# Kernel optimization log

Hardware: AMD Instinct MI355X
Metric: run time of the kernel (lower is better)

## Reference

```python
import jax, jax.numpy as jnp
import numpy as np

TEMPERATURE = 0.07
EPS = 1e-8  # torch CosineSimilarity eps


def setup_inputs() -> dict:
    key = jax.random.key(0)
    features = jax.random.normal(key, (16, 1024, 512), dtype=jnp.float32)
    return {"features": features}


def reference(features):
    """Vectorized equivalent of the original double Python loop.

    For each b and each t in [1, T-2]:
      anchor = f[b,t], positive = f[b,t+1]
      negatives = all frames j with j < t-1 or j >= t+2  (excludes t-1, t, t+1)
      loss_bt = -log( exp(cos(a,p)/T) / (exp(cos(a,p)/T) + sum_j exp(cos(a,n_j)/T)) )
    Returns mean over all (b, t) pairs (neg pool is non-empty for all t when T > 3).
    """
    B, T, D = features.shape
    norm = jnp.maximum(jnp.linalg.norm(features, axis=-1, keepdims=True), EPS)
    n = features / norm  # [B, T, D]
    # full pairwise cosine-sim logits, scaled by temperature
    sim = jnp.einsum('btd,bsd->bts', n, n) / TEMPERATURE  # [B, T, T]

    t_idx = jnp.arange(1, T - 1)            # anchors t = 1 .. T-2
    j_idx = jnp.arange(T)
    # negatives: j in [0, t-1) union [t+2, T)  -> excludes t-1, t, t+1
    neg_mask = (j_idx[None, :] < t_idx[:, None] - 1) | (j_idx[None, :] >= t_idx[:, None] + 2)  # [T-2, T]

    logits = sim[:, 1:T - 1, :]                                   # [B, T-2, T]
    pos = logits[:, jnp.arange(T - 2), jnp.arange(2, T)]          # sim[b, t, t+1] -> [B, T-2]
    neg_logits = jnp.where(neg_mask[None], logits, -jnp.inf)
    lse_neg = jax.nn.logsumexp(neg_logits, axis=-1)               # log sum_j exp(neg_sim)
    # -log(exp(pos)/(exp(pos)+negsum)) = logaddexp(pos, lse_neg) - pos
    loss_bt = jnp.logaddexp(pos, lse_neg) - pos                   # [B, T-2]
    return jnp.mean(loss_bt)
```

## Files before the change

kernel.cpp:

```cpp
#include <hip/hip_runtime.h>
#include <hip/hip_bf16.h>
#include <hip/hip_fp8.h>

#define B_ 16
#define T_ 1024
#define D_ 512
#define EPS_ 1e-8f
#define SCALE2 20.609929155566063f
#define LN2_ 0.6931471805599453f

#define BT 64
#define NB 16
#define NPAIR (NB * (NB + 1) / 2)
#define NKIT 4
#define SCL 0x7B7B7B7B

typedef __attribute__((ext_vector_type(4))) int   int4v;
typedef __attribute__((ext_vector_type(8))) int   int8v;
typedef __attribute__((ext_vector_type(4))) float floatx4;

typedef __attribute__((address_space(1))) const unsigned int g_u32;
typedef __attribute__((address_space(3))) unsigned int l_u32;

__device__ __forceinline__ void glds16(const void* g, void* l) {
    __builtin_amdgcn_global_load_lds((g_u32*)g, (l_u32*)l, 16, 0, 0);
}

__device__ __forceinline__ unsigned char f2e4m3(float x) {
    __hip_fp8_e4m3 q(x);
    return (unsigned char)q.__x;
}

__global__ __launch_bounds__(256) void norm_kernel(const float* __restrict__ f,
                                                   unsigned char* __restrict__ nrm,
                                                   float* __restrict__ rs_g,
                                                   float* __restrict__ rp_g,
                                                   float* __restrict__ out) {
    const int gi = blockIdx.x * 256 + threadIdx.x;
    if (gi < B_ * T_) { rs_g[gi] = 0.0f; rp_g[gi] = 0.0f; }
    if (gi == 0) out[0] = 0.0f;

    const int row  = blockIdx.x * 4 + (threadIdx.x >> 6);
    const int lane = threadIdx.x & 63;
    const size_t off = (size_t)row * D_ + lane * 8;
    const float4 v0 = *(const float4*)(f + off);
    const float4 v1 = *(const float4*)(f + off + 4);
    float ss = v0.x*v0.x + v0.y*v0.y + v0.z*v0.z + v0.w*v0.w
             + v1.x*v1.x + v1.y*v1.y + v1.z*v1.z + v1.w*v1.w;
    #pragma unroll
    for (int o = 32; o >= 1; o >>= 1) ss += __shfl_xor(ss, o, 64);
    const float sc = 16.0f / fmaxf(sqrtf(ss), EPS_);
    unsigned int w0 =  (unsigned int)f2e4m3(v0.x*sc)
                    | ((unsigned int)f2e4m3(v0.y*sc) << 8)
                    | ((unsigned int)f2e4m3(v0.z*sc) << 16)
                    | ((unsigned int)f2e4m3(v0.w*sc) << 24);
    unsigned int w1 =  (unsigned int)f2e4m3(v1.x*sc)
                    | ((unsigned int)f2e4m3(v1.y*sc) << 8)
                    | ((unsigned int)f2e4m3(v1.z*sc) << 16)
                    | ((unsigned int)f2e4m3(v1.w*sc) << 24);
    uint2 w; w.x = w0; w.y = w1;
    *(uint2*)(nrm + (size_t)row * D_ + lane * 8) = w;
}

__global__ __launch_bounds__(64) void loss_kernel(const unsigned char* __restrict__ nrm,
                                                  float* __restrict__ rs_g,
                                                  float* __restrict__ rp_g) {
    const int slot = blockIdx.x & 15;
    int u = blockIdx.x >> 4;
    const int b = ((slot & 7) << 1) | (slot >> 3);
    int bi = 0, rem = NB;
    while (u >= rem) { u -= rem; --rem; ++bi; }
    const int bj   = bi + u;
    const bool diag = (bi == bj);
    const bool near = (bj - bi) <= 1;

    const int t0 = bi * BT;
    const int j0 = bj * BT;
    const char* base = (const char*)(nrm + (size_t)b * T_ * D_);

    __shared__ __align__(16) char Ar[4][4096];
    __shared__ __align__(16) char Br[4][4096];

    const int l = threadIdx.x & 63;
    const int m = l & 15;

    const int r   = l >> 2;
    const int gsw = (l & 3) ^ ((r >> 1) & 3);
    const char* sA[4];
    const char* sB[4];
    #pragma unroll
    for (int i = 0; i < 4; ++i) {
        sA[i] = base + (size_t)(t0 + i * 16 + r) * 512 + gsw * 16;
        sB[i] = base + (size_t)(j0 + i * 16 + r) * 512 + gsw * 16;
    }

#define ISSUE(S) do {                                                  \
    _Pragma("unroll")                                                  \
    for (int i_ = 0; i_ < 4; ++i_)                                     \
        glds16(sA[i_] + (S) * 64, Ar[(S) & 3] + i_ * 1024);            \
    if (!diag) {                                                       \
        _Pragma("unroll")                                              \
        for (int i_ = 0; i_ < 4; ++i_)                                 \
            glds16(sB[i_] + (S) * 64, Br[(S) & 3] + i_ * 1024);        \
    }                                                                  \
} while (0)

    const int kqh  = l >> 5;
    const int ph0  = (2 * ((l >> 4) & 1)) ^ ((m >> 1) & 3);
    const int rd0  = m * 64 + ph0 * 16;
    const int rd1  = m * 64 + (ph0 ^ 1) * 16;

    floatx4 acc[4][4] = {};

    ISSUE(0); ISSUE(1);

    #pragma unroll
    for (int j = 0; j < NKIT; ++j) {
        __syncthreads();
        if (j < NKIT - 1) { ISSUE(2 * j + 2); ISSUE(2 * j + 3); }

        const char* As = Ar[(2 * j + kqh) & 3];
        const char* Bs = diag ? Ar[(2 * j + kqh) & 3] : Br[(2 * j + kqh) & 3];
        int8v af[4], bf[4];
        #pragma unroll
        for (int mi = 0; mi < 4; ++mi) {
            int4v lo = *(const int4v*)(As + mi * 1024 + rd0);
            int4v hi = *(const int4v*)(As + mi * 1024 + rd1);
            af[mi] = __builtin_shufflevector(lo, hi, 0, 1, 2, 3, 4, 5, 6, 7);
        }
        #pragma unroll
        for (int ni = 0; ni < 4; ++ni) {
            int4v lo = *(const int4v*)(Bs + ni * 1024 + rd0);
            int4v hi = *(const int4v*)(Bs + ni * 1024 + rd1);
            bf[ni] = __builtin_shufflevector(lo, hi, 0, 1, 2, 3, 4, 5, 6, 7);
        }

        #pragma unroll
        for (int mi = 0; mi < 4; ++mi)
            #pragma unroll
            for (int ni = 0; ni < 4; ++ni)
                acc[mi][ni] = __builtin_amdgcn_mfma_scale_f32_16x16x128_f8f6f4(
                    af[mi], bf[ni], acc[mi][ni],
                    0, 0,
                    0, SCL,
                    0, SCL);
    }
#undef ISSUE

    const int lrow = l >> 4;
    const int lcol = l & 15;
    const int bT   = b * T_;
    float cs[4] = {0.f, 0.f, 0.f, 0.f};

    #pragma unroll
    for (int mi = 0; mi < 4; ++mi) {
        #pragma unroll
        for (int rg = 0; rg < 4; ++rg) {
            const int t = t0 + mi * 16 + lrow * 4 + rg;
            float rsum = 0.f;
            #pragma unroll
            for (int ni = 0; ni < 4; ++ni) {
                const int j  = j0 + ni * 16 + lcol;
                const float s2 = acc[mi][ni][rg] * SCALE2;
                const float e  = exp2f(s2);
                if (j < t - 1 || j > t + 1) { rsum += e; cs[ni] += e; }
                if (near && j == t + 1) atomicAdd(&rp_g[bT + t], s2);
            }
            #pragma unroll
            for (int o = 8; o >= 1; o >>= 1) rsum += __shfl_xor(rsum, o, 64);
            if (lcol == 0) atomicAdd(&rs_g[bT + t], rsum);
        }
    }
    if (!diag) {
        #pragma unroll
        for (int ni = 0; ni < 4; ++ni) {
            float c = cs[ni];
            c += __shfl_xor(c, 16, 64);
            c += __shfl_xor(c, 32, 64);
            if (lrow == 0)
                atomicAdd(&rs_g[bT + j0 + ni * 16 + lcol], c);
        }
    }
}

__global__ __launch_bounds__(256) void fin_kernel(const float* __restrict__ rs_g,
                                                  const float* __restrict__ rp_g,
                                                  float* __restrict__ out) {
    const int idx = blockIdx.x * 256 + threadIdx.x;
    float v = 0.0f;
    if (idx < B_ * T_) {
        const int t = idx & (T_ - 1);
        if (t >= 1 && t <= T_ - 2) {
            const float p2 = rp_g[idx];
            const float s  = rs_g[idx];
            v = (log2f(exp2f(p2) + s) - p2) * LN2_;
        }
    }
    #pragma unroll
    for (int o = 32; o >= 1; o >>= 1) v += __shfl_xor(v, o, 64);
    __shared__ float ws_[4];
    if ((threadIdx.x & 63) == 0) ws_[threadIdx.x >> 6] = v;
    __syncthreads();
    if (threadIdx.x == 0) {
        const float scale = 1.0f / (float)(B_ * (T_ - 2));
        atomicAdd(out, (ws_[0] + ws_[1] + ws_[2] + ws_[3]) * scale);
    }
}

extern "C" void kernel_launch(void* const* d_in, const int* in_sizes, int n_in,
                              void* d_out, int out_size, void* d_ws, size_t ws_size,
                              hipStream_t stream) {
    const float* feat = (const float*)d_in[0];
    float* out = (float*)d_out;

    unsigned char* nrm = (unsigned char*)d_ws;
    float* rs_g = (float*)((char*)d_ws + (size_t)B_ * T_ * D_);
    float* rp_g = rs_g + B_ * T_;

    norm_kernel<<<B_ * T_ / 4, 256, 0, stream>>>(feat, nrm, rs_g, rp_g, out);
    loss_kernel<<<NPAIR * B_, 64, 0, stream>>>(nrm, rs_g, rp_g);
    fin_kernel<<<(B_ * T_ + 255) / 256, 256, 0, stream>>>(rs_g, rp_g, out);
}
```

Before: 99.59 us.

## Load MFMA fragments directly from global into registers, dropping LDS staging

```diff
diff --git a/kernel.cpp b/kernel.cpp
--- a/kernel.cpp
+++ b/kernel.cpp
@@ -1,5 +1,4 @@
 #include <hip/hip_runtime.h>
-#include <hip/hip_bf16.h>
 #include <hip/hip_fp8.h>
 
 #define B_ 16
@@ -12,19 +11,10 @@
 #define BT 64
 #define NB 16
 #define NPAIR (NB * (NB + 1) / 2)
-#define NKIT 4
 #define SCL 0x7B7B7B7B
 
-typedef __attribute__((ext_vector_type(4))) int   int4v;
 typedef __attribute__((ext_vector_type(8))) int   int8v;
 typedef __attribute__((ext_vector_type(4))) float floatx4;
-
-typedef __attribute__((address_space(1))) const unsigned int g_u32;
-typedef __attribute__((address_space(3))) unsigned int l_u32;
-
-__device__ __forceinline__ void glds16(const void* g, void* l) {
-    __builtin_amdgcn_global_load_lds((g_u32*)g, (l_u32*)l, 16, 0, 0);
-}
 
 __device__ __forceinline__ unsigned char f2e4m3(float x) {
     __hip_fp8_e4m3 q(x);
@@ -62,9 +52,9 @@
     *(uint2*)(nrm + (size_t)row * D_ + lane * 8) = w;
 }
 
-__global__ __launch_bounds__(64) void loss_kernel(const unsigned char* __restrict__ nrm,
-                                                  float* __restrict__ rs_g,
-                                                  float* __restrict__ rp_g) {
+__global__ __launch_bounds__(64, 2) void loss_kernel(const unsigned char* __restrict__ nrm,
+                                                     float* __restrict__ rs_g,
+                                                     float* __restrict__ rp_g) {
     const int slot = blockIdx.x & 15;
     int u = blockIdx.x >> 4;
     const int b = ((slot & 7) << 1) | (slot >> 3);
@@ -78,74 +68,52 @@
     const int j0 = bj * BT;
     const char* base = (const char*)(nrm + (size_t)b * T_ * D_);
 
-    __shared__ __align__(16) char Ar[4][4096];
-    __shared__ __align__(16) char Br[4][4096];
+    const int l  = threadIdx.x & 63;
+    const int m  = l & 15;
+    const int kq = l >> 4;
 
-    const int l = threadIdx.x & 63;
-    const int m = l & 15;
-
-    const int r   = l >> 2;
-    const int gsw = (l & 3) ^ ((r >> 1) & 3);
-    const char* sA[4];
-    const char* sB[4];
+    const char* pA[4];
+    const char* pB[4];
     #pragma unroll
     for (int i = 0; i < 4; ++i) {
-        sA[i] = base + (size_t)(t0 + i * 16 + r) * 512 + gsw * 16;
-        sB[i] = base + (size_t)(j0 + i * 16 + r) * 512 + gsw * 16;
+        pA[i] = base + (size_t)(t0 + i * 16 + m) * 512 + kq * 32;
+        pB[i] = base + (size_t)(j0 + i * 16 + m) * 512 + kq * 32;
     }
 
-#define ISSUE(S) do {                                                  \
+    floatx4 acc[4][4] = {};
+    int8v a0[4], b0[4], a1[4], b1[4];
+
+#define LK(dA, dB, kk) do {                                            \
     _Pragma("unroll")                                                  \
     for (int i_ = 0; i_ < 4; ++i_)                                     \
-        glds16(sA[i_] + (S) * 64, Ar[(S) & 3] + i_ * 1024);            \
-    if (!diag) {                                                       \
-        _Pragma("unroll")                                              \
-        for (int i_ = 0; i_ < 4; ++i_)                                 \
-            glds16(sB[i_] + (S) * 64, Br[(S) & 3] + i_ * 1024);        \
-    }                                                                  \
+        dA[i_] = *(const int8v*)(pA[i_] + (kk) * 128);                 \
+    _Pragma("unroll")                                                  \
+    for (int i_ = 0; i_ < 4; ++i_)                                     \
+        dB[i_] = *(const int8v*)(pB[i_] + (kk) * 128);                 \
 } while (0)
 
-    const int kqh  = l >> 5;
-    const int ph0  = (2 * ((l >> 4) & 1)) ^ ((m >> 1) & 3);
-    const int rd0  = m * 64 + ph0 * 16;
-    const int rd1  = m * 64 + (ph0 ^ 1) * 16;
+#define MM(aF, bF) do {                                                \
+    _Pragma("unroll")                                                  \
+    for (int mi_ = 0; mi_ < 4; ++mi_)                                  \
+        _Pragma("unroll")                                              \
+        for (int ni_ = 0; ni_ < 4; ++ni_)                              \
+            acc[mi_][ni_] = __builtin_amdgcn_mfma_scale_f32_16x16x128_f8f6f4( \
+                aF[mi_], bF[ni_], acc[mi_][ni_],                       \
+                0, 0,               \
+                0, SCL,             \
+                0, SCL);            \
+} while (0)
 
-    floatx4 acc[4][4] = {};
-
-    ISSUE(0); ISSUE(1);
-
-    #pragma unroll
-    for (int j = 0; j < NKIT; ++j) {
-        __syncthreads();
-        if (j < NKIT - 1) { ISSUE(2 * j + 2); ISSUE(2 * j + 3); }
-
-        const char* As = Ar[(2 * j + kqh) & 3];
-        const char* Bs = diag ? Ar[(2 * j + kqh) & 3] : Br[(2 * j + kqh) & 3];
-        int8v af[4], bf[4];
-        #pragma unroll
-        for (int mi = 0; mi < 4; ++mi) {
-            int4v lo = *(const int4v*)(As + mi * 1024 + rd0);
-            int4v hi = *(const int4v*)(As + mi * 1024 + rd1);
-            af[mi] = __builtin_shufflevector(lo, hi, 0, 1, 2, 3, 4, 5, 6, 7);
-        }
-        #pragma unroll
-        for (int ni = 0; ni < 4; ++ni) {
-            int4v lo = *(const int4v*)(Bs + ni * 1024 + rd0);
-            int4v hi = *(const int4v*)(Bs + ni * 1024 + rd1);
-            bf[ni] = __builtin_shufflevector(lo, hi, 0, 1, 2, 3, 4, 5, 6, 7);
-        }
-
-        #pragma unroll
-        for (int mi = 0; mi < 4; ++mi)
-            #pragma unroll
-            for (int ni = 0; ni < 4; ++ni)
-                acc[mi][ni] = __builtin_amdgcn_mfma_scale_f32_16x16x128_f8f6f4(
-                    af[mi], bf[ni], acc[mi][ni],
-                    0, 0,
-                    0, SCL,
-                    0, SCL);
-    }
-#undef ISSUE
+    LK(a0, b0, 0);
+    LK(a1, b1, 1);
+    MM(a0, b0);
+    LK(a0, b0, 2);
+    MM(a1, b1);
+    LK(a1, b1, 3);
+    MM(a0, b0);
+    MM(a1, b1);
+#undef LK
+#undef MM
 
     const int lrow = l >> 4;
     const int lcol = l & 15;
```

After: 109.1 us. 9.5% more time.

## Use 128x128 tiles with four waves per block in loss kernel

Applied to the files above, without the earlier changes.

```diff
diff --git a/kernel.cpp b/kernel.cpp
--- a/kernel.cpp
+++ b/kernel.cpp
@@ -1,5 +1,4 @@
 #include <hip/hip_runtime.h>
-#include <hip/hip_bf16.h>
 #include <hip/hip_fp8.h>
 
 #define B_ 16
@@ -9,9 +8,9 @@
 #define SCALE2 20.609929155566063f
 #define LN2_ 0.6931471805599453f
 
-#define BT 64
-#define NB 16
-#define NPAIR (NB * (NB + 1) / 2)
+#define BT2 128
+#define NB2 8
+#define NPAIR2 (NB2 * (NB2 + 1) / 2)
 #define NKIT 4
 #define SCL 0x7B7B7B7B
 
@@ -62,53 +61,56 @@
     *(uint2*)(nrm + (size_t)row * D_ + lane * 8) = w;
 }
 
-__global__ __launch_bounds__(64) void loss_kernel(const unsigned char* __restrict__ nrm,
-                                                  float* __restrict__ rs_g,
-                                                  float* __restrict__ rp_g) {
+__global__ __launch_bounds__(256, 2) void loss_kernel(const unsigned char* __restrict__ nrm,
+                                                      float* __restrict__ rs_g,
+                                                      float* __restrict__ rp_g) {
     const int slot = blockIdx.x & 15;
     int u = blockIdx.x >> 4;
     const int b = ((slot & 7) << 1) | (slot >> 3);
-    int bi = 0, rem = NB;
+    int bi = 0, rem = NB2;
     while (u >= rem) { u -= rem; --rem; ++bi; }
     const int bj   = bi + u;
     const bool diag = (bi == bj);
-    const bool near = (bj - bi) <= 1;
-
-    const int t0 = bi * BT;
-    const int j0 = bj * BT;
+
+    const int t0 = bi * BT2;
+    const int j0 = bj * BT2;
     const char* base = (const char*)(nrm + (size_t)b * T_ * D_);
 
-    __shared__ __align__(16) char Ar[4][4096];
-    __shared__ __align__(16) char Br[4][4096];
-
-    const int l = threadIdx.x & 63;
-    const int m = l & 15;
+    __shared__ __align__(16) char Ar[4][8192];
+    __shared__ __align__(16) char Br[4][8192];
+
+    const int l  = threadIdx.x & 63;
+    const int w  = threadIdx.x >> 6;
+    const int wr = w >> 1;
+    const int wc = w & 1;
+    const int m  = l & 15;
+    const bool dead = diag && (w == 2);
 
     const int r   = l >> 2;
     const int gsw = (l & 3) ^ ((r >> 1) & 3);
-    const char* sA[4];
-    const char* sB[4];
-    #pragma unroll
-    for (int i = 0; i < 4; ++i) {
-        sA[i] = base + (size_t)(t0 + i * 16 + r) * 512 + gsw * 16;
-        sB[i] = base + (size_t)(j0 + i * 16 + r) * 512 + gsw * 16;
-    }
-
-#define ISSUE(S) do {                                                  \
-    _Pragma("unroll")                                                  \
-    for (int i_ = 0; i_ < 4; ++i_)                                     \
-        glds16(sA[i_] + (S) * 64, Ar[(S) & 3] + i_ * 1024);            \
-    if (!diag) {                                                       \
-        _Pragma("unroll")                                              \
-        for (int i_ = 0; i_ < 4; ++i_)                                 \
-            glds16(sB[i_] + (S) * 64, Br[(S) & 3] + i_ * 1024);        \
-    }                                                                  \
+    const char* sAq[2];
+    const char* sBq[2];
+    #pragma unroll
+    for (int q = 0; q < 2; ++q) {
+        sAq[q] = base + (size_t)(t0 + (2 * w + q) * 16 + r) * 512 + gsw * 16;
+        sBq[q] = base + (size_t)(j0 + (2 * w + q) * 16 + r) * 512 + gsw * 16;
+    }
+
+#define ISSUE(S) do {                                                      \
+    _Pragma("unroll")                                                      \
+    for (int q_ = 0; q_ < 2; ++q_)                                         \
+        glds16(sAq[q_] + (S) * 64, Ar[(S) & 3] + (2 * w + q_) * 1024);     \
+    if (!diag) {                                                           \
+        _Pragma("unroll")                                                  \
+        for (int q_ = 0; q_ < 2; ++q_)                                     \
+            glds16(sBq[q_] + (S) * 64, Br[(S) & 3] + (2 * w + q_) * 1024); \
+    }                                                                      \
 } while (0)
 
-    const int kqh  = l >> 5;
-    const int ph0  = (2 * ((l >> 4) & 1)) ^ ((m >> 1) & 3);
-    const int rd0  = m * 64 + ph0 * 16;
-    const int rd1  = m * 64 + (ph0 ^ 1) * 16;
+    const int kqh = l >> 5;
+    const int ph0 = (2 * ((l >> 4) & 1)) ^ ((m >> 1) & 3);
+    const int rd0 = m * 64 + ph0 * 16;
+    const int rd1 = m * 64 + (ph0 ^ 1) * 16;
 
     floatx4 acc[4][4] = {};
 
@@ -119,34 +121,42 @@
         __syncthreads();
         if (j < NKIT - 1) { ISSUE(2 * j + 2); ISSUE(2 * j + 3); }
 
-        const char* As = Ar[(2 * j + kqh) & 3];
-        const char* Bs = diag ? Ar[(2 * j + kqh) & 3] : Br[(2 * j + kqh) & 3];
-        int8v af[4], bf[4];
-        #pragma unroll
-        for (int mi = 0; mi < 4; ++mi) {
-            int4v lo = *(const int4v*)(As + mi * 1024 + rd0);
-            int4v hi = *(const int4v*)(As + mi * 1024 + rd1);
-            af[mi] = __builtin_shufflevector(lo, hi, 0, 1, 2, 3, 4, 5, 6, 7);
-        }
-        #pragma unroll
-        for (int ni = 0; ni < 4; ++ni) {
-            int4v lo = *(const int4v*)(Bs + ni * 1024 + rd0);
-            int4v hi = *(const int4v*)(Bs + ni * 1024 + rd1);
-            bf[ni] = __builtin_shufflevector(lo, hi, 0, 1, 2, 3, 4, 5, 6, 7);
-        }
-
-        #pragma unroll
-        for (int mi = 0; mi < 4; ++mi)
-            #pragma unroll
-            for (int ni = 0; ni < 4; ++ni)
-                acc[mi][ni] = __builtin_amdgcn_mfma_scale_f32_16x16x128_f8f6f4(
-                    af[mi], bf[ni], acc[mi][ni],
-                    0, 0,
-                    0, SCL,
-                    0, SCL);
+        if (!dead) {
+            const char* As = Ar[(2 * j + kqh) & 3] + wr * 4096;
+            const char* Bs = (diag ? Ar[(2 * j + kqh) & 3] : Br[(2 * j + kqh) & 3]) + wc * 4096;
+            int8v af[4], bf[4];
+            #pragma unroll
+            for (int mi = 0; mi < 4; ++mi) {
+                int4v lo = *(const int4v*)(As + mi * 1024 + rd0);
+                int4v hi = *(const int4v*)(As + mi * 1024 + rd1);
+                af[mi] = __builtin_shufflevector(lo, hi, 0, 1, 2, 3, 4, 5, 6, 7);
+            }
+            #pragma unroll
+            for (int ni = 0; ni < 4; ++ni) {
+                int4v lo = *(const int4v*)(Bs + ni * 1024 + rd0);
+                int4v hi = *(const int4v*)(Bs + ni * 1024 + rd1);
+                bf[ni] = __builtin_shufflevector(lo, hi, 0, 1, 2, 3, 4, 5, 6, 7);
+            }
+            #pragma unroll
+            for (int mi = 0; mi < 4; ++mi)
+                #pragma unroll
+                for (int ni = 0; ni < 4; ++ni)
+                    acc[mi][ni] = __builtin_amdgcn_mfma_scale_f32_16x16x128_f8f6f4(
+                        af[mi], bf[ni], acc[mi][ni],
+                        0, 0,
+                        0, SCL,
+                        0, SCL);
+        }
     }
 #undef ISSUE
 
+    if (dead) return;
+
+    const int t0q = t0 + wr * 64;
+    const int j0q = j0 + wc * 64;
+    const int d   = t0q - j0q;
+    const bool nearq   = (d >= -64 && d <= 62);
+    const bool cols_on = !(diag && (wr == wc));
     const int lrow = l >> 4;
     const int lcol = l & 15;
     const int bT   = b * T_;
@@ -156,29 +166,29 @@
     for (int mi = 0; mi < 4; ++mi) {
         #pragma unroll
         for (int rg = 0; rg < 4; ++rg) {
-            const int t = t0 + mi * 16 + lrow * 4 + rg;
+            const int t = t0q + mi * 16 + lrow * 4 + rg;
             float rsum = 0.f;
             #pragma unroll
             for (int ni = 0; ni < 4; ++ni) {
-                const int j  = j0 + ni * 16 + lcol;
+                const int j  = j0q + ni * 16 + lcol;
                 const float s2 = acc[mi][ni][rg] * SCALE2;
                 const float e  = exp2f(s2);
                 if (j < t - 1 || j > t + 1) { rsum += e; cs[ni] += e; }
-                if (near && j == t + 1) atomicAdd(&rp_g[bT + t], s2);
+                if (nearq && j == t + 1) atomicAdd(&rp_g[bT + t], s2);
             }
             #pragma unroll
             for (int o = 8; o >= 1; o >>= 1) rsum += __shfl_xor(rsum, o, 64);
             if (lcol == 0) atomicAdd(&rs_g[bT + t], rsum);
         }
     }
-    if (!diag) {
+    if (cols_on) {
         #pragma unroll
         for (int ni = 0; ni < 4; ++ni) {
             float c = cs[ni];
             c += __shfl_xor(c, 16, 64);
             c += __shfl_xor(c, 32, 64);
             if (lrow == 0)
-                atomicAdd(&rs_g[bT + j0 + ni * 16 + lcol], c);
+                atomicAdd(&rs_g[bT + j0q + ni * 16 + lcol], c);
         }
     }
 }
@@ -218,6 +228,6 @@
     float* rp_g = rs_g + B_ * T_;
 
     norm_kernel<<<B_ * T_ / 4, 256, 0, stream>>>(feat, nrm, rs_g, rp_g, out);
-    loss_kernel<<<NPAIR * B_, 64, 0, stream>>>(nrm, rs_g, rp_g);
+    loss_kernel<<<NPAIR2 * B_, 256, 0, stream>>>(nrm, rs_g, rp_g);
     fin_kernel<<<(B_ * T_ + 255) / 256, 256, 0, stream>>>(rs_g, rp_g, out);
 }
```

After: 93.24 us. -6.4%, faster.
